# Kernel tuning notes

Measured on AMD Instinct MI355X. Metric: run time of the kernel, lower is better.

Reference implementation:

```python
import jax, jax.numpy as jnp
import numpy as np

NEG_SLOPE = 0.2  # PyG GATv2Conv default negative_slope


def gatv2(x, edge_index, w_l, w_r, att, bias):
    # x: [G, N, F]  (G = batch*step independent graphs sharing edge_index)
    G, N, F = x.shape
    H, C = att.shape
    # add self loops (PyG default add_self_loops=True)
    loops = jnp.arange(N, dtype=edge_index.dtype)
    src = jnp.concatenate([edge_index[0], loops])  # [E]
    dst = jnp.concatenate([edge_index[1], loops])  # [E]
    # linear projections for source / target nodes
    x_l = (x @ w_l).reshape(G, N, H, C)  # source projection
    x_r = (x @ w_r).reshape(G, N, H, C)  # target projection
    # gather along edges -> [E, G, H, C] (edge axis leading for segment ops)
    src_f = jnp.take(x_l, src, axis=1).transpose(1, 0, 2, 3)
    dst_f = jnp.take(x_r, dst, axis=1).transpose(1, 0, 2, 3)
    # GATv2 attention logit: a^T leaky_relu(W_l x_j + W_r x_i)
    e = jax.nn.leaky_relu(src_f + dst_f, NEG_SLOPE)
    logit = jnp.einsum('eghc,hc->egh', e, att)  # [E, G, H]
    # numerically-stable segment softmax over incoming edges per dst node
    m = jax.ops.segment_max(logit, dst, num_segments=N)  # [N, G, H]
    ex = jnp.exp(logit - m[dst])
    denom = jax.ops.segment_sum(ex, dst, num_segments=N)  # [N, G, H]
    alpha = ex / denom[dst]  # [E, G, H]
    # weighted scatter-add aggregation
    out = jax.ops.segment_sum(alpha[..., None] * src_f, dst, num_segments=N)  # [N,G,H,C]
    out = out.transpose(1, 0, 2, 3).reshape(G, N, H * C) + bias
    return out


def setup_inputs() -> dict:
    key = jax.random.key(0)
    ks = jax.random.split(key, 6)
    B, T, N, F = 8, 10, 1000, 64
    E, H, C = 8000, 1, 64
    x = jax.random.normal(ks[0], (B, T, N, F), dtype=jnp.float32)
    edge_index = jax.random.randint(ks[1], (2, E), 0, N, dtype=jnp.int64)
    s = 1.0 / np.sqrt(F)
    w_l = jax.random.normal(ks[2], (F, H * C), dtype=jnp.float32) * s
    w_r = jax.random.normal(ks[3], (F, H * C), dtype=jnp.float32) * s
    att = jax.random.normal(ks[4], (H, C), dtype=jnp.float32) * (1.0 / np.sqrt(C))
    bias = jnp.zeros((H * C,), dtype=jnp.float32)
    return {"x": x, "edge_index": edge_index, "w_l": w_l, "w_r": w_r, "att": att, "bias": bias}


def reference(x, edge_index, w_l, w_r, att, bias):
    B, T, N, F = x.shape
    out = gatv2(x.reshape(B * T, N, F), edge_index, w_l, w_r, att, bias)
    return out.reshape(B, T, N, -1)
```

## Files before the change

### kernel.cpp

```cpp
#include <hip/hip_runtime.h>
#include <hip/hip_bf16.h>


#define GG 80
#define NN 1000
#define EE 8000
#define MM 80000
#define PAD 40
#define NEG_SLOPE 0.2f

typedef __attribute__((ext_vector_type(8))) short short8;
typedef __attribute__((ext_vector_type(4))) float floatx4;

__device__ __forceinline__ unsigned short f2b(float f) {
    unsigned int u = __float_as_uint(f);
    unsigned int r = u + 0x7fffu + ((u >> 16) & 1u);
    return (unsigned short)(r >> 16);
}

__global__ __launch_bounds__(256) void proj_csr_kernel(
    const float* __restrict__ x,
    const float* __restrict__ wl,
    const float* __restrict__ wr,
    const int* __restrict__ ei32,
    unsigned short* __restrict__ XLt,
    unsigned short* __restrict__ XRt,
    int* __restrict__ list2)
{
    __shared__ __align__(16) unsigned short Wt[128 * 72];
    __shared__ int cnt[1024];
    const int t = threadIdx.x;

    if (blockIdx.x == 313) {
        int oddw = ei32[2 * t + 1];
        const int stride = __any(oddw != 0) ? 1 : 2;

        for (int i = t; i < 1024; i += 256) cnt[i] = 0;
        __syncthreads();

        int dv[32], sv[32];
#pragma unroll
        for (int k = 0; k < 32; k++) {
            int e = t + (k << 8);
            dv[k] = (e < EE) ? ei32[(size_t)(EE + e) * stride] : -1;
        }
#pragma unroll
        for (int k = 0; k < 32; k++) {
            int e = t + (k << 8);
            sv[k] = (e < EE) ? ei32[(size_t)e * stride] : 0;
        }
#pragma unroll
        for (int k = 0; k < 32; k++) {
            if (dv[k] >= 0) {
                int pos = atomicAdd(&cnt[dv[k]], 1);
                if (pos < PAD - 2) list2[dv[k] * PAD + 1 + pos] = sv[k];
            }
        }
        __syncthreads();
        for (int n = t; n < NN; n += 256) {
            int c = min(cnt[n], PAD - 2);
            list2[n * PAD + 1 + c] = n;
            list2[n * PAD] = c + 1;
        }
        return;
    }

    for (int idx = t; idx < 8192; idx += 256) {
        int half = idx >> 12;
        int k = (idx & 4095) >> 6;
        int c = idx & 63;
        float v = half ? wr[k * 64 + c] : wl[k * 64 + c];
        Wt[(c + half * 64) * 72 + k] = f2b(v);
    }
    __syncthreads();

    const int wave = t >> 6;
    const int lane = t & 63;
    const int quad = lane >> 4;
    const int lm   = lane & 15;
    const int Rb   = (blockIdx.x * 4 + wave) * 64;

    short8 Bf[2][8];
#pragma unroll
    for (int ks = 0; ks < 2; ks++)
#pragma unroll
        for (int sub = 0; sub < 8; sub++)
            Bf[ks][sub] = *(const short8*)(&Wt[(sub * 16 + lm) * 72 + ks * 32 + quad * 8]);

    const float4* x4 = (const float4*)x;

#pragma unroll
    for (int sm = 0; sm < 4; sm++) {
        const int rbase = Rb + sm * 16;
        const int r  = rbase + lm;
        const int rc = (r < MM) ? r : (MM - 1);

        short8 Af[2];
#pragma unroll
        for (int ks = 0; ks < 2; ks++) {
            float4 p = x4[(size_t)rc * 16 + ks * 8 + quad * 2];
            float4 q = x4[(size_t)rc * 16 + ks * 8 + quad * 2 + 1];
            short8 a;
            a[0] = (short)f2b(p.x); a[1] = (short)f2b(p.y);
            a[2] = (short)f2b(p.z); a[3] = (short)f2b(p.w);
            a[4] = (short)f2b(q.x); a[5] = (short)f2b(q.y);
            a[6] = (short)f2b(q.z); a[7] = (short)f2b(q.w);
            Af[ks] = a;
        }

        floatx4 acc[8];
#pragma unroll
        for (int sub = 0; sub < 8; sub++) acc[sub] = (floatx4)(0.f);
#pragma unroll
        for (int ks = 0; ks < 2; ks++)
#pragma unroll
            for (int sub = 0; sub < 8; sub++)
                acc[sub] = __builtin_amdgcn_mfma_f32_16x16x32_bf16(Af[ks], Bf[ks][sub], acc[sub], 0, 0, 0);

#pragma unroll
        for (int reg = 0; reg < 4; reg++) {
            int rr = rbase + quad * 4 + reg;
            if (rr < MM) {
                int g = rr / 1000;
                int n = rr - g * 1000;
                size_t ob = ((size_t)n * GG + g) * 64 + lm;
#pragma unroll
                for (int sub = 0; sub < 4; sub++)
                    XLt[ob + sub * 16] = f2b(acc[sub][reg]);
#pragma unroll
                for (int sub = 4; sub < 8; sub++)
                    XRt[ob + (sub - 4) * 16] = f2b(acc[sub][reg]);
            }
        }
    }
}

__global__ __launch_bounds__(128) void agg_kernel(
    const unsigned short* __restrict__ XLt,
    const unsigned short* __restrict__ XRt,
    const int* __restrict__ list2,
    const float* __restrict__ att,
    const float* __restrict__ bias,
    float* __restrict__ out)
{
    __shared__ int sh[PAD];
    const int t = threadIdx.x;
    const int d = blockIdx.x;
    const int g = blockIdx.y * 16 + (t >> 3);
    const int cg = t & 7;

    if (t < PAD) sh[t] = list2[d * PAD + t];

    float xr[8], av[8], bv[8];
    {
        const uint4 u = *(const uint4*)(XRt + ((size_t)d * GG + g) * 64 + cg * 8);
        const unsigned int uw[4] = {u.x, u.y, u.z, u.w};
#pragma unroll
        for (int q = 0; q < 4; q++) {
            xr[2 * q + 0] = __uint_as_float(uw[q] << 16);
            xr[2 * q + 1] = __uint_as_float(uw[q] & 0xffff0000u);
        }
#pragma unroll
        for (int j = 0; j < 8; j++) { av[j] = att[cg * 8 + j]; bv[j] = bias[cg * 8 + j]; }
    }
    __syncthreads();
    const int cnt = sh[0];

    float acc[8];
#pragma unroll
    for (int j = 0; j < 8; j++) acc[j] = 0.f;
    float dn = 0.f;

    for (int i = 0; i < cnt; i += 16) {
        uint4 u[16];
#pragma unroll
        for (int e = 0; e < 16; e++) {
            int idx = i + e;
            int s = sh[1 + ((idx < cnt) ? idx : 0)];
            u[e] = *(const uint4*)(XLt + ((size_t)s * GG + g) * 64 + cg * 8);
        }
#pragma unroll
        for (int e = 0; e < 16; e++) {
            const unsigned int uw[4] = {u[e].x, u[e].y, u[e].z, u[e].w};
            float xf[8];
#pragma unroll
            for (int q = 0; q < 4; q++) {
                xf[2 * q]     = __uint_as_float(uw[q] << 16);
                xf[2 * q + 1] = __uint_as_float(uw[q] & 0xffff0000u);
            }
            float p = 0.f;
#pragma unroll
            for (int j = 0; j < 8; j++) {
                float v = xf[j] + xr[j];
                float lv = fmaxf(v, 0.f) + NEG_SLOPE * fminf(v, 0.f);
                p = fmaf(av[j], lv, p);
            }
            p += __shfl_xor(p, 1, 64);
            p += __shfl_xor(p, 2, 64);
            p += __shfl_xor(p, 4, 64);
            float w = (i + e < cnt) ? __expf(p) : 0.f;
            dn += w;
#pragma unroll
            for (int j = 0; j < 8; j++) acc[j] = fmaf(w, xf[j], acc[j]);
        }
    }

    const float inv = 1.f / dn;
    float4 r0, r1;
    r0.x = acc[0] * inv + bv[0];
    r0.y = acc[1] * inv + bv[1];
    r0.z = acc[2] * inv + bv[2];
    r0.w = acc[3] * inv + bv[3];
    r1.x = acc[4] * inv + bv[4];
    r1.y = acc[5] * inv + bv[5];
    r1.z = acc[6] * inv + bv[6];
    r1.w = acc[7] * inv + bv[7];
    float* po = out + ((size_t)g * NN + d) * 64 + cg * 8;
    *(float4*)po = r0;
    *(float4*)(po + 4) = r1;
}

extern "C" void kernel_launch(void* const* d_in, const int* in_sizes, int n_in,
                              void* d_out, int out_size, void* d_ws, size_t ws_size,
                              hipStream_t stream) {
    const float* x    = (const float*)d_in[0];
    const int*   ei   = (const int*)d_in[1];
    const float* wl   = (const float*)d_in[2];
    const float* wr   = (const float*)d_in[3];
    const float* att  = (const float*)d_in[4];
    const float* bias = (const float*)d_in[5];
    float* out = (float*)d_out;

    char* ws = (char*)d_ws;
    int* list2 = (int*)ws;
    unsigned short* XLt = (unsigned short*)(ws + 262144);
    unsigned short* XRt = XLt + (size_t)NN * GG * 64;

    hipLaunchKernelGGL(proj_csr_kernel, dim3(314), dim3(256), 0, stream,
                       x, wl, wr, ei, XLt, XRt, list2);
    hipLaunchKernelGGL(agg_kernel, dim3(NN, 5), dim3(128), 0, stream,
                       XLt, XRt, list2, att, bias, out);
}
```

Before: 113.5 us.

## Stage per-graph source features in LDS and aggregate many destinations per block

The aggregation kernel now assigns each block one graph (and a third of the destination nodes), first copying that graph's whole XL projection (1000x64 bf16, padded) into 144KB of shared memory. Neighbor gathers then read from LDS instead of scattered global loads, and adjacency indices are loaded per lane and broadcast with shuffles. The leaky-relu dot is also rewritten as two fmas. The cost is a large dynamic LDS allocation, which allows only one block per CU and a small grid of 240 blocks, plus redundant staging across the three y-blocks per graph.

```diff
diff --git a/kernel.cpp b/kernel.cpp
--- a/kernel.cpp
+++ b/kernel.cpp
@@ -135,7 +135,7 @@
     }
 }
 
-__global__ __launch_bounds__(128) void agg_kernel(
+__global__ __launch_bounds__(512) void agg_kernel(
     const unsigned short* __restrict__ XLt,
     const unsigned short* __restrict__ XRt,
     const int* __restrict__ list2,
@@ -143,81 +143,114 @@
     const float* __restrict__ bias,
     float* __restrict__ out)
 {
-    __shared__ int sh[PAD];
+    extern __shared__ unsigned short sXL[];
     const int t = threadIdx.x;
-    const int d = blockIdx.x;
-    const int g = blockIdx.y * 16 + (t >> 3);
+    const int g = blockIdx.x;
+    const int lane = t & 63;
+    const int base = lane & ~7;
     const int cg = t & 7;
-
-    if (t < PAD) sh[t] = list2[d * PAD + t];
-
-    float xr[8], av[8], bv[8];
-    {
-        const uint4 u = *(const uint4*)(XRt + ((size_t)d * GG + g) * 64 + cg * 8);
-        const unsigned int uw[4] = {u.x, u.y, u.z, u.w};
-#pragma unroll
-        for (int q = 0; q < 4; q++) {
-            xr[2 * q + 0] = __uint_as_float(uw[q] << 16);
-            xr[2 * q + 1] = __uint_as_float(uw[q] & 0xffff0000u);
-        }
-#pragma unroll
-        for (int j = 0; j < 8; j++) { av[j] = att[cg * 8 + j]; bv[j] = bias[cg * 8 + j]; }
+    const int octg = t >> 3;
+
+#pragma unroll
+    for (int i = 0; i < 16; i++) {
+        int n = i * 64 + octg;
+        if (n < NN) {
+            uint4 v = *(const uint4*)(XLt + ((size_t)n * GG + g) * 64 + cg * 8);
+            *(uint4*)(&sXL[n * 72 + cg * 8]) = v;
+        }
+    }
+
+    float av[8], avn[8], bv[8];
+#pragma unroll
+    for (int j = 0; j < 8; j++) {
+        av[j]  = att[cg * 8 + j];
+        avn[j] = av[j] * NEG_SLOPE;
+        bv[j]  = bias[cg * 8 + j];
     }
     __syncthreads();
-    const int cnt = sh[0];
-
-    float acc[8];
-#pragma unroll
-    for (int j = 0; j < 8; j++) acc[j] = 0.f;
-    float dn = 0.f;
-
-    for (int i = 0; i < cnt; i += 16) {
-        uint4 u[16];
-#pragma unroll
-        for (int e = 0; e < 16; e++) {
-            int idx = i + e;
-            int s = sh[1 + ((idx < cnt) ? idx : 0)];
-            u[e] = *(const uint4*)(XLt + ((size_t)s * GG + g) * 64 + cg * 8);
-        }
-#pragma unroll
-        for (int e = 0; e < 16; e++) {
-            const unsigned int uw[4] = {u[e].x, u[e].y, u[e].z, u[e].w};
-            float xf[8];
+
+    const int dstart = blockIdx.y * 334;
+    const int dend   = min(dstart + 334, NN);
+
+    for (int d = dstart + octg; d < dend; d += 64) {
+        int hv = list2[d * PAD + cg];
+        uint4 uxr = *(const uint4*)(XRt + ((size_t)d * GG + g) * 64 + cg * 8);
+        int cnt = __shfl(hv, base, 64);
+        cnt = min(cnt, PAD - 1);
+
+        float xr[8];
+        {
+            const unsigned int uw[4] = {uxr.x, uxr.y, uxr.z, uxr.w};
 #pragma unroll
             for (int q = 0; q < 4; q++) {
-                xf[2 * q]     = __uint_as_float(uw[q] << 16);
-                xf[2 * q + 1] = __uint_as_float(uw[q] & 0xffff0000u);
-            }
-            float p = 0.f;
+                xr[2 * q]     = __uint_as_float(uw[q] << 16);
+                xr[2 * q + 1] = __uint_as_float(uw[q] & 0xffff0000u);
+            }
+        }
+
+        float acc[8];
+#pragma unroll
+        for (int j = 0; j < 8; j++) acc[j] = 0.f;
+        float dn = 0.f;
+
+        int lo = 0, nsrc = 7, joff = 1;
+        for (int b = 0; lo < cnt; b++) {
+            if (b > 0) {
+                hv = list2[d * PAD + b * 8 + cg];
+                nsrc = 8; joff = 0;
+            }
+            uint4 u[8];
 #pragma unroll
             for (int j = 0; j < 8; j++) {
-                float v = xf[j] + xr[j];
-                float lv = fmaxf(v, 0.f) + NEG_SLOPE * fminf(v, 0.f);
-                p = fmaf(av[j], lv, p);
-            }
-            p += __shfl_xor(p, 1, 64);
-            p += __shfl_xor(p, 2, 64);
-            p += __shfl_xor(p, 4, 64);
-            float w = (i + e < cnt) ? __expf(p) : 0.f;
-            dn += w;
-#pragma unroll
-            for (int j = 0; j < 8; j++) acc[j] = fmaf(w, xf[j], acc[j]);
-        }
-    }
-
-    const float inv = 1.f / dn;
-    float4 r0, r1;
-    r0.x = acc[0] * inv + bv[0];
-    r0.y = acc[1] * inv + bv[1];
-    r0.z = acc[2] * inv + bv[2];
-    r0.w = acc[3] * inv + bv[3];
-    r1.x = acc[4] * inv + bv[4];
-    r1.y = acc[5] * inv + bv[5];
-    r1.z = acc[6] * inv + bv[6];
-    r1.w = acc[7] * inv + bv[7];
-    float* po = out + ((size_t)g * NN + d) * 64 + cg * 8;
-    *(float4*)po = r0;
-    *(float4*)(po + 4) = r1;
+                if (j < nsrc) {
+                    int sl = __shfl(hv, base + joff + j, 64);
+                    int s = (lo + j < cnt) ? sl : 0;
+                    u[j] = *(const uint4*)(&sXL[s * 72 + cg * 8]);
+                }
+            }
+#pragma unroll
+            for (int j = 0; j < 8; j++) {
+                if (j < nsrc) {
+                    const unsigned int uw[4] = {u[j].x, u[j].y, u[j].z, u[j].w};
+                    float xf[8];
+#pragma unroll
+                    for (int q = 0; q < 4; q++) {
+                        xf[2 * q]     = __uint_as_float(uw[q] << 16);
+                        xf[2 * q + 1] = __uint_as_float(uw[q] & 0xffff0000u);
+                    }
+                    float p = 0.f;
+#pragma unroll
+                    for (int c = 0; c < 8; c++) {
+                        float v = xf[c] + xr[c];
+                        p = fmaf(av[c], fmaxf(v, 0.f), p);
+                        p = fmaf(avn[c], fminf(v, 0.f), p);
+                    }
+                    p += __shfl_xor(p, 1, 64);
+                    p += __shfl_xor(p, 2, 64);
+                    p += __shfl_xor(p, 4, 64);
+                    float w = (lo + j < cnt) ? __expf(p) : 0.f;
+                    dn += w;
+#pragma unroll
+                    for (int c = 0; c < 8; c++) acc[c] = fmaf(w, xf[c], acc[c]);
+                }
+            }
+            lo += nsrc;
+        }
+
+        const float inv = 1.f / dn;
+        float4 r0, r1;
+        r0.x = acc[0] * inv + bv[0];
+        r0.y = acc[1] * inv + bv[1];
+        r0.z = acc[2] * inv + bv[2];
+        r0.w = acc[3] * inv + bv[3];
+        r1.x = acc[4] * inv + bv[4];
+        r1.y = acc[5] * inv + bv[5];
+        r1.z = acc[6] * inv + bv[6];
+        r1.w = acc[7] * inv + bv[7];
+        float* po = out + ((size_t)g * NN + d) * 64 + cg * 8;
+        *(float4*)po = r0;
+        *(float4*)(po + 4) = r1;
+    }
 }
 
 extern "C" void kernel_launch(void* const* d_in, const int* in_sizes, int n_in,
@@ -238,6 +271,6 @@
 
     hipLaunchKernelGGL(proj_csr_kernel, dim3(314), dim3(256), 0, stream,
                        x, wl, wr, ei, XLt, XRt, list2);
-    hipLaunchKernelGGL(agg_kernel, dim3(NN, 5), dim3(128), 0, stream,
+    hipLaunchKernelGGL(agg_kernel, dim3(GG, 3), dim3(512), 144000, stream,
                        XLt, XRt, list2, att, bias, out);
 }
```

Result: slower. 116.1 us (+2.3%).
